# Kernel tuning notes

Hardware: AMD Instinct MI355X
Metric: run time of the kernel (lower is better)

## Reference

```python
import jax, jax.numpy as jnp
import numpy as np

H = 16
D_MODEL = 1024
HEAD_DIM = D_MODEL // H
NEG = -1e9


def setup_inputs() -> dict:
    key = jax.random.key(0)
    k1, k2, k3, k4, k5, k6 = jax.random.split(key, 6)
    B, L = 2, 2048
    feature = jax.random.normal(k1, (B, L, D_MODEL), dtype=jnp.float32)
    mask = jax.random.randint(k2, (B, L), 0, 2, dtype=jnp.int32)
    # Linear weights stored torch-style as [out, in]; biases zero-init per initialize().
    s = 1.0 / np.sqrt(D_MODEL)
    W_Q = jax.random.uniform(k3, (D_MODEL, D_MODEL), jnp.float32, -s, s)
    W_K = jax.random.uniform(k4, (D_MODEL, D_MODEL), jnp.float32, -s, s)
    W_V = jax.random.uniform(k5, (D_MODEL, D_MODEL), jnp.float32, -s, s)
    b_Q = jnp.zeros((D_MODEL,), jnp.float32)
    b_K = jnp.zeros((D_MODEL,), jnp.float32)
    b_V = jnp.zeros((D_MODEL,), jnp.float32)
    return {"feature": feature, "mask": mask, "W_Q": W_Q, "b_Q": b_Q,
            "W_K": W_K, "b_K": b_K, "W_V": W_V, "b_V": b_V}


def reference(feature, mask, W_Q, b_Q, W_K, b_K, W_V, b_V):
    B, L, _ = feature.shape
    scale = jnp.sqrt(jnp.float32(HEAD_DIM))
    # Projections: torch Linear is x @ W^T + b. Split into heads: [B, H, L, Dh]
    def proj(W, b):
        y = feature @ W.T + b
        return y.reshape(B, L, H, HEAD_DIM).transpose(0, 2, 1, 3)
    Q = proj(W_Q, b_Q)
    K = proj(W_K, b_K)
    V = proj(W_V, b_V)
    # Scores [B, H, Lq, Lk]
    A = jnp.einsum('bhqd,bhkd->bhqk', Q, K) / scale
    # Key-side mask broadcast over heads and query positions
    A = jnp.where(mask[:, None, None, :] == 0, jnp.float32(NEG), A)
    alpha = jax.nn.softmax(A, axis=-1)
    out = jnp.einsum('bhqk,bhkd->bhqd', alpha, V)  # [B, H, L, Dh]
    return out.transpose(0, 2, 1, 3).reshape(B, L, H * HEAD_DIM)
```

## Files before the change

### kernel.cpp

```cpp
#include <hip/hip_runtime.h>

typedef __bf16 bf16;
typedef __attribute__((ext_vector_type(4))) __bf16 bf16x4;
typedef __attribute__((ext_vector_type(8))) __bf16 bf16x8;
typedef __attribute__((ext_vector_type(4))) float f32x4;
typedef __attribute__((ext_vector_type(16))) float f32x16;
typedef unsigned int u32;

#define D_MODEL 1024
#define SEQ_L   2048
#define NHEAD   16
#define HDIM    64
#define MROWS   4096

#define FEAT_OFF  512u
#define WQ_OFF    (FEAT_OFF + 4194304u)
#define WK_OFF    (WQ_OFF + 1048576u)
#define WV_OFF    (WK_OFF + 1048576u)
#define BQ_OFF    (WV_OFF + 1048576u)
#define BK_OFF    (BQ_OFF + 1024u)
#define BV_OFF    (BK_OFF + 1024u)
#define Q_OFF     (BV_OFF + 1024u)
#define K_OFF     (Q_OFF + 4194304u)
#define V_OFF     (K_OFF + 4194304u)

typedef const __attribute__((address_space(1))) u32* gp_t;
typedef __attribute__((address_space(3))) u32* lp_t;
__device__ __forceinline__ void ld16(const bf16* g, bf16* l) {
    __builtin_amdgcn_global_load_lds((gp_t)g, (lp_t)l, 16, 0, 0);
}

__global__ void convert_in(const float* __restrict__ feat,
                           const float* __restrict__ wq, const float* __restrict__ wk,
                           const float* __restrict__ wv,
                           const float* __restrict__ bq, const float* __restrict__ bk,
                           const float* __restrict__ bv,
                           bf16* __restrict__ ws) {
    const int bid = blockIdx.x;
    const float* src; bf16* dst; int off;
    if (bid < 4096)      { src = feat; dst = ws + FEAT_OFF; off = bid * 1024; }
    else if (bid < 5120) { src = wq;   dst = ws + WQ_OFF;   off = (bid - 4096) * 1024; }
    else if (bid < 6144) { src = wk;   dst = ws + WK_OFF;   off = (bid - 5120) * 1024; }
    else if (bid < 7168) { src = wv;   dst = ws + WV_OFF;   off = (bid - 6144) * 1024; }
    else if (bid == 7168){ src = bq;   dst = ws + BQ_OFF;   off = 0; }
    else if (bid == 7169){ src = bk;   dst = ws + BK_OFF;   off = 0; }
    else                 { src = bv;   dst = ws + BV_OFF;   off = 0; }
    int idx = off + threadIdx.x * 4;
    float4 v = *(const float4*)(src + idx);
    dst[idx + 0] = (bf16)v.x;
    dst[idx + 1] = (bf16)v.y;
    dst[idx + 2] = (bf16)v.z;
    dst[idx + 3] = (bf16)v.w;
}

__global__ __launch_bounds__(256, 2) void qkv_gemm(const bf16* __restrict__ ws,
                                                   bf16* __restrict__ wsw,
                                                   const int* __restrict__ mask) {
    const int zi = blockIdx.z;
    const bf16* Amat = (zi == 2) ? ws + WV_OFF : ws + FEAT_OFF;
    const bf16* Bmat = (zi == 0) ? ws + WQ_OFF : (zi == 1) ? ws + WK_OFF : ws + FEAT_OFF;
    const bf16* bias = ws + ((zi == 0) ? BQ_OFF : (zi == 1) ? BK_OFF : BV_OFF);
    bf16* Y = (zi == 2) ? wsw + V_OFF : wsw + Q_OFF + (size_t)zi * 4194304u;

    __shared__ bf16 Alds[128 * 64];
    __shared__ bf16 Blds[128 * 64];

    const int t    = threadIdx.x;
    const int lane = t & 63;
    const int wave = t >> 6;
    const int quad = lane >> 4;
    const int l16  = lane & 15;
    const int m0   = ((zi == 2) ? blockIdx.y : blockIdx.x) * 128;
    const int n0   = ((zi == 2) ? blockIdx.x : blockIdx.y) * 128;
    const int wrow = (wave >> 1) * 64;
    const int wcol = (wave & 1) * 64;

    const int r8 = lane >> 3;
    const int sl = lane & 7;
    const int sg = sl ^ r8;

    f32x4 acc[4][4];
    for (int mi = 0; mi < 4; ++mi)
        for (int ni = 0; ni < 4; ++ni)
            acc[mi][ni] = (f32x4){0.f, 0.f, 0.f, 0.f};

    for (int k0 = 0; k0 < D_MODEL; k0 += 64) {
#pragma unroll
        for (int i = 0; i < 4; ++i) {
            int ch  = wave * 4 + i;
            int row = ch * 8 + r8;
            ld16(Amat + (size_t)(m0 + row) * D_MODEL + k0 + sg * 8, Alds + ch * 512);
            ld16(Bmat + (size_t)(n0 + row) * D_MODEL + k0 + sg * 8, Blds + ch * 512);
        }
        __syncthreads();

#pragma unroll
        for (int kk = 0; kk < 2; ++kk) {
            const int sgb = quad + kk * 4;
            bf16x8 af[4], bfr[4];
#pragma unroll
            for (int mi = 0; mi < 4; ++mi) {
                int row = wrow + mi * 16 + l16;
                af[mi] = *(const bf16x8*)(&Alds[row * 64 + ((sgb ^ (row & 7)) << 3)]);
            }
#pragma unroll
            for (int ni = 0; ni < 4; ++ni) {
                int row = wcol + ni * 16 + l16;
                bfr[ni] = *(const bf16x8*)(&Blds[row * 64 + ((sgb ^ (row & 7)) << 3)]);
            }
#pragma unroll
            for (int mi = 0; mi < 4; ++mi)
#pragma unroll
                for (int ni = 0; ni < 4; ++ni)
                    acc[mi][ni] = __builtin_amdgcn_mfma_f32_16x16x32_bf16(
                        af[mi], bfr[ni], acc[mi][ni], 0, 0, 0);
        }
        __syncthreads();
    }

    if (zi < 2) {
#pragma unroll
        for (int ni = 0; ni < 4; ++ni) {
            int col = n0 + wcol + ni * 16 + l16;
            float bvf = (float)bias[col];
#pragma unroll
            for (int mi = 0; mi < 4; ++mi) {
                int rowb = m0 + wrow + mi * 16 + quad * 4;
#pragma unroll
                for (int r = 0; r < 4; ++r) {
                    float v = acc[mi][ni][r] + bvf;
                    if (zi == 1 && mask[rowb + r] == 0) v = 0.f;
                    Y[(size_t)(rowb + r) * D_MODEL + col] = (bf16)v;
                }
            }
        }
    } else {
#pragma unroll
        for (int mi = 0; mi < 4; ++mi) {
#pragma unroll
            for (int r = 0; r < 4; ++r) {
                int rowv = m0 + wrow + mi * 16 + quad * 4 + r;
                float bvf = (float)bias[rowv];
#pragma unroll
                for (int ni = 0; ni < 4; ++ni) {
                    int col = n0 + wcol + ni * 16 + l16;
                    float v = acc[mi][ni][r] + bvf;
                    if (mask[col] == 0) v = 0.f;
                    size_t addr = (size_t)(col >> 11) * 2097152u +
                                  (size_t)rowv * 2048u + (col & 2047);
                    Y[addr] = (bf16)v;
                }
            }
        }
    }
}

__global__ __launch_bounds__(128, 4) void attn_kernel(
    const bf16* __restrict__ ws, bf16* __restrict__ wsw,
    const int* __restrict__ mask, float* __restrict__ out) {
    const int bh  = blockIdx.x;
    const int qt  = blockIdx.y;
    const int ks2 = blockIdx.z;
    const int b   = bh >> 4, h = bh & 15;
    const int t    = threadIdx.x;
    const int lane = t & 63;
    const int wave = t >> 6;
    const int half = lane >> 5;
    const int l31  = lane & 31;
    const int kt0  = ks2 * 1024;

    __shared__ bf16 Klds[64 * 64];
    __shared__ bf16 Vlds[64 * 64];

    const bf16* Qh  = ws + Q_OFF + (size_t)(b * SEQ_L) * D_MODEL + h * HDIM;
    const bf16* Kh  = ws + K_OFF + (size_t)(b * SEQ_L) * D_MODEL + h * HDIM;
    const bf16* Vth = ws + V_OFF + (size_t)b * 2097152u + (size_t)(h * HDIM) * SEQ_L;

    const int qrow0 = qt * 64 + wave * 32;
    bf16x8 qf[4];
#pragma unroll
    for (int ks = 0; ks < 4; ++ks) {
        qf[ks] = *(const bf16x8*)(Qh + (size_t)(qrow0 + l31) * D_MODEL
                                  + ks * 16 + half * 8);
#pragma unroll
        for (int j = 0; j < 8; ++j)
            qf[ks][j] = (bf16)((float)qf[ks][j] * 0.125f);
    }

    f32x16 o[2];
    float lsum = 0.f;
    int nm = 0;
#pragma unroll
    for (int dt = 0; dt < 2; ++dt)
#pragma unroll
        for (int i = 0; i < 16; ++i) o[dt][i] = 0.f;

    const int srow = (lane >> 3);
    const int sg   = (lane & 7) ^ srow;

    for (int kt = kt0; kt < kt0 + 1024; kt += 64) {
#pragma unroll
        for (int i = 0; i < 4; ++i) {
            int row = i * 16 + wave * 8 + srow;
            ld16(Kh + (size_t)(kt + row) * D_MODEL + sg * 8,
                 Klds + i * 1024 + wave * 512);
            ld16(Vth + (size_t)row * SEQ_L + kt + sg * 8,
                 Vlds + i * 1024 + wave * 512);
        }
        int mv = mask[b * SEQ_L + kt + lane];
        nm += (int)__popcll(__ballot(mv != 0));
        __syncthreads();

        f32x16 st[2];
#pragma unroll
        for (int ktile = 0; ktile < 2; ++ktile) {
#pragma unroll
            for (int i = 0; i < 16; ++i) st[ktile][i] = 0.f;
#pragma unroll
            for (int ks = 0; ks < 4; ++ks) {
                const int row  = ktile * 32 + l31;
                const int slot = (ks * 2 + half) ^ (l31 & 7);
                bf16x8 kf = *(const bf16x8*)(&Klds[row * 64 + slot * 8]);
                st[ktile] = __builtin_amdgcn_mfma_f32_32x32x16_bf16(
                    kf, qf[ks], st[ktile], 0, 0, 0);
            }
        }

        bf16x4 pk[2][4];
#pragma unroll
        for (int ktile = 0; ktile < 2; ++ktile) {
#pragma unroll
            for (int g = 0; g < 4; ++g) {
                bf16x4 pkv;
#pragma unroll
                for (int j = 0; j < 4; ++j) {
                    float p = __expf(st[ktile][g * 4 + j]);
                    lsum += p;
                    pkv[j] = (bf16)p;
                }
                pk[ktile][g] = pkv;
            }
        }

        bf16x8 pf[4];
#pragma unroll
        for (int ks = 0; ks < 4; ++ks) {
            const int k1 = ks & 1, kt2 = ks >> 1;
            uint2 a  = __builtin_bit_cast(uint2, pk[kt2][2 * k1]);
            uint2 bb = __builtin_bit_cast(uint2, pk[kt2][2 * k1 + 1]);
            uint2 keep, send;
            keep.x = half ? bb.x : a.x;  keep.y = half ? bb.y : a.y;
            send.x = half ? a.x : bb.x;  send.y = half ? a.y : bb.y;
            uint2 recv;
            recv.x = (unsigned)__shfl_xor((int)send.x, 32);
            recv.y = (unsigned)__shfl_xor((int)send.y, 32);
            uint4 frag;
            frag.x = half ? recv.x : keep.x;
            frag.y = half ? recv.y : keep.y;
            frag.z = half ? keep.x : recv.x;
            frag.w = half ? keep.y : recv.y;
            pf[ks] = __builtin_bit_cast(bf16x8, frag);
        }

#pragma unroll
        for (int dt = 0; dt < 2; ++dt) {
#pragma unroll
            for (int ks = 0; ks < 4; ++ks) {
                const int row  = dt * 32 + l31;
                const int slot = (ks * 2 + half) ^ (l31 & 7);
                bf16x8 vf = *(const bf16x8*)(&Vlds[row * 64 + slot * 8]);
                o[dt] = __builtin_amdgcn_mfma_f32_32x32x16_bf16(
                    pf[ks], vf, o[dt], 0, 0, 0);
            }
        }
        __syncthreads();
    }

    float* Lp  = (float*)(wsw + WQ_OFF);
    bf16*  O1  = wsw + FEAT_OFF;
    float l = lsum + __shfl_xor(lsum, 32) - (float)(1024 - nm);
    if (half == 0)
        Lp[ks2 * 65536 + bh * 2048 + qrow0 + l31] = l;
#pragma unroll
    for (int r = 0; r < 16; ++r) {
        const int q32 = (r & 3) + 8 * (r >> 2) + 4 * half;
        const int q = qrow0 + q32;
        const size_t base = ((size_t)(b * SEQ_L + q)) * D_MODEL + h * HDIM;
        if (ks2 == 0) {
            out[base + l31]      = o[0][r];
            out[base + 32 + l31] = o[1][r];
        } else {
            O1[base + l31]      = (bf16)o[0][r];
            O1[base + 32 + l31] = (bf16)o[1][r];
        }
    }
}

__global__ void combine(float* __restrict__ out, const bf16* __restrict__ ws) {
    const float* Lp = (const float*)(ws + WQ_OFF);
    const bf16*  O1 = ws + FEAT_OFF;
    int idx = (blockIdx.x * 256 + threadIdx.x) * 4;
    int row = idx >> 10;
    int col = idx & 1023;
    int b = row >> 11, q = row & 2047, h = col >> 6;
    int li = (b * 16 + h) * 2048 + q;
    float rl = 1.0f / fmaxf(Lp[li] + Lp[65536 + li], 1e-30f);
    float4 o0 = *(float4*)(out + idx);
    bf16x4 o1 = *(const bf16x4*)(O1 + idx);
    float4 res;
    res.x = (o0.x + (float)o1[0]) * rl;
    res.y = (o0.y + (float)o1[1]) * rl;
    res.z = (o0.z + (float)o1[2]) * rl;
    res.w = (o0.w + (float)o1[3]) * rl;
    *(float4*)(out + idx) = res;
}

extern "C" void kernel_launch(void* const* d_in, const int* in_sizes, int n_in,
                              void* d_out, int out_size, void* d_ws, size_t ws_size,
                              hipStream_t stream) {
    const float* feat = (const float*)d_in[0];
    const int*   mask = (const int*)d_in[1];
    const float* Wq = (const float*)d_in[2];
    const float* bq = (const float*)d_in[3];
    const float* Wk = (const float*)d_in[4];
    const float* bk = (const float*)d_in[5];
    const float* Wv = (const float*)d_in[6];
    const float* bv = (const float*)d_in[7];

    bf16* ws = (bf16*)d_ws;

    convert_in<<<7171, 256, 0, stream>>>(feat, Wq, Wk, Wv, bq, bk, bv, ws);

    dim3 g1(32, 8, 3);
    qkv_gemm<<<g1, 256, 0, stream>>>(ws, ws, mask);

    dim3 g2(2 * NHEAD, SEQ_L / 64, 2);
    attn_kernel<<<g2, 128, 0, stream>>>(ws, ws, mask, (float*)d_out);

    combine<<<4096, 256, 0, stream>>>((float*)d_out, ws);
}
```

Baseline: 183.0 us.

## Fold softmax scale into W_Q conversion, use exp2 and MFMA row-sum

Pre-multiplies W_Q and b_Q by 0.125·log2(e) during the fp32→bf16 conversion, which removes the per-row Q scaling in the attention kernel and lets raw exp2 replace __expf. The softmax denominator now comes from an extra MFMA against a ones vector, computed from the bf16-rounded probabilities, instead of scalar adds plus a cross-half shuffle. This lowers VALU work in the inner loop at the cost of four extra MFMAs per tile, and the scale is applied before bf16 rounding of the weights rather than after the projection.

```diff
diff --git a/kernel.cpp b/kernel.cpp
--- a/kernel.cpp
+++ b/kernel.cpp
@@ -12,6 +12,8 @@
 #define NHEAD   16
 #define HDIM    64
 #define MROWS   4096
+
+#define S_SCALE 0.18033688f
 
 #define FEAT_OFF  512u
 #define WQ_OFF    (FEAT_OFF + 4194304u)
@@ -37,20 +39,20 @@
                            const float* __restrict__ bv,
                            bf16* __restrict__ ws) {
     const int bid = blockIdx.x;
-    const float* src; bf16* dst; int off;
+    const float* src; bf16* dst; int off; float sc = 1.0f;
     if (bid < 4096)      { src = feat; dst = ws + FEAT_OFF; off = bid * 1024; }
-    else if (bid < 5120) { src = wq;   dst = ws + WQ_OFF;   off = (bid - 4096) * 1024; }
+    else if (bid < 5120) { src = wq;   dst = ws + WQ_OFF;   off = (bid - 4096) * 1024; sc = S_SCALE; }
     else if (bid < 6144) { src = wk;   dst = ws + WK_OFF;   off = (bid - 5120) * 1024; }
     else if (bid < 7168) { src = wv;   dst = ws + WV_OFF;   off = (bid - 6144) * 1024; }
-    else if (bid == 7168){ src = bq;   dst = ws + BQ_OFF;   off = 0; }
+    else if (bid == 7168){ src = bq;   dst = ws + BQ_OFF;   off = 0; sc = S_SCALE; }
     else if (bid == 7169){ src = bk;   dst = ws + BK_OFF;   off = 0; }
     else                 { src = bv;   dst = ws + BV_OFF;   off = 0; }
     int idx = off + threadIdx.x * 4;
     float4 v = *(const float4*)(src + idx);
-    dst[idx + 0] = (bf16)v.x;
-    dst[idx + 1] = (bf16)v.y;
-    dst[idx + 2] = (bf16)v.z;
-    dst[idx + 3] = (bf16)v.w;
+    dst[idx + 0] = (bf16)(v.x * sc);
+    dst[idx + 1] = (bf16)(v.y * sc);
+    dst[idx + 2] = (bf16)(v.z * sc);
+    dst[idx + 3] = (bf16)(v.w * sc);
 }
 
 __global__ __launch_bounds__(256, 2) void qkv_gemm(const bf16* __restrict__ ws,
@@ -179,21 +181,18 @@
     const int qrow0 = qt * 64 + wave * 32;
     bf16x8 qf[4];
 #pragma unroll
-    for (int ks = 0; ks < 4; ++ks) {
+    for (int ks = 0; ks < 4; ++ks)
         qf[ks] = *(const bf16x8*)(Qh + (size_t)(qrow0 + l31) * D_MODEL
                                   + ks * 16 + half * 8);
-#pragma unroll
-        for (int j = 0; j < 8; ++j)
-            qf[ks][j] = (bf16)((float)qf[ks][j] * 0.125f);
-    }
-
-    f32x16 o[2];
-    float lsum = 0.f;
+
+    bf16x8 ones;
+#pragma unroll
+    for (int j = 0; j < 8; ++j) ones[j] = (bf16)1.0f;
+
+    f32x16 o[2], lacc;
     int nm = 0;
 #pragma unroll
-    for (int dt = 0; dt < 2; ++dt)
-#pragma unroll
-        for (int i = 0; i < 16; ++i) o[dt][i] = 0.f;
+    for (int i = 0; i < 16; ++i) { o[0][i] = 0.f; o[1][i] = 0.f; lacc[i] = 0.f; }
 
     const int srow = (lane >> 3);
     const int sg   = (lane & 7) ^ srow;
@@ -233,11 +232,8 @@
             for (int g = 0; g < 4; ++g) {
                 bf16x4 pkv;
 #pragma unroll
-                for (int j = 0; j < 4; ++j) {
-                    float p = __expf(st[ktile][g * 4 + j]);
-                    lsum += p;
-                    pkv[j] = (bf16)p;
-                }
+                for (int j = 0; j < 4; ++j)
+                    pkv[j] = (bf16)__builtin_amdgcn_exp2f(st[ktile][g * 4 + j]);
                 pk[ktile][g] = pkv;
             }
         }
@@ -263,6 +259,9 @@
         }
 
 #pragma unroll
+        for (int ks = 0; ks < 4; ++ks)
+            lacc = __builtin_amdgcn_mfma_f32_32x32x16_bf16(pf[ks], ones, lacc, 0, 0, 0);
+#pragma unroll
         for (int dt = 0; dt < 2; ++dt) {
 #pragma unroll
             for (int ks = 0; ks < 4; ++ks) {
@@ -278,14 +277,14 @@
 
     float* Lp  = (float*)(wsw + WQ_OFF);
     bf16*  O1  = wsw + FEAT_OFF;
-    float l = lsum + __shfl_xor(lsum, 32) - (float)(1024 - nm);
-    if (half == 0)
-        Lp[ks2 * 65536 + bh * 2048 + qrow0 + l31] = l;
+    const float corr = (float)(1024 - nm);
 #pragma unroll
     for (int r = 0; r < 16; ++r) {
         const int q32 = (r & 3) + 8 * (r >> 2) + 4 * half;
         const int q = qrow0 + q32;
         const size_t base = ((size_t)(b * SEQ_L + q)) * D_MODEL + h * HDIM;
+        if (l31 == 0)
+            Lp[ks2 * 65536 + bh * 2048 + qrow0 + q32] = lacc[r] - corr;
         if (ks2 == 0) {
             out[base + l31]      = o[0][r];
             out[base + 32 + l31] = o[1][r];
```

Measured after the change: 177.3 us. 1.03x faster.
